# Performance work log

Hardware: AMD Instinct MI355X
Metric: run time of the kernel (lower is better)

Reference implementation:

```python
import jax, jax.numpy as jnp
import numpy as np

EMBEDDING_DIM = 256
WINDOW = 3


def setup_inputs() -> dict:
    key = jax.random.key(0)
    ks = jax.random.split(key, 7)
    B, T, F = 65536, 16, 129
    D = 64  # feature_dim = embedding_dim // 4 = cutoff = int(F*0.5)
    freq_history = jax.random.normal(ks[0], (B, T, F), dtype=jnp.float32)
    # pattern_detector: Linear(D, D) + LayerNorm(D) + GELU
    W1 = jax.random.normal(ks[1], (D, D), dtype=jnp.float32) * (1.0 / np.sqrt(D))
    b1 = jnp.zeros((D,), dtype=jnp.float32)
    gamma = jnp.ones((D,), dtype=jnp.float32)
    beta = jnp.zeros((D,), dtype=jnp.float32)
    # repetition_classifier: Linear(D, 1) + Sigmoid
    W2 = jax.random.normal(ks[2], (D, 1), dtype=jnp.float32) * (1.0 / np.sqrt(D))
    b2 = jnp.zeros((1,), dtype=jnp.float32)
    return {"freq_history": freq_history, "W1": W1, "b1": b1,
            "gamma": gamma, "beta": beta, "W2": W2, "b2": b2}


def reference(freq_history, W1, b1, gamma, beta, W2, b2):
    F = freq_history.shape[2]
    cutoff = int(F * 0.5)  # 64
    # keep last `window_size` steps
    fh = freq_history[:, -WINDOW:, :]  # [B, 3, F]
    # high-frequency magnitude: abs -> clamp -> per-sample standardize -> clamp
    hfm = jnp.clip(jnp.abs(fh[:, :, :cutoff]), 1e-5, 10.0)  # [B, 3, C]
    mean = hfm.mean(axis=(1, 2), keepdims=True)
    std = hfm.std(axis=(1, 2), keepdims=True, ddof=1) + 1e-5  # torch std is unbiased
    hfm = jnp.clip((hfm - mean) / std, -3.0, 3.0)
    # pattern detector on latest frame (dim_adapter is None: input_dim == feature_dim)
    latest = hfm[:, -1, :]  # [B, C]
    h = latest @ W1 + b1
    mu = h.mean(axis=-1, keepdims=True)
    var = h.var(axis=-1, keepdims=True)
    h = (h - mu) * jax.lax.rsqrt(var + 1e-5) * gamma + beta
    h = jax.nn.gelu(h, approximate=False)  # torch default GELU is exact erf
    repetition_scores = jax.nn.sigmoid(h @ W2 + b2)  # [B, 1]
    # DTW similarity: sequences passed have length 1 -> short-circuit branch:
    # dist = ||first - last||_2, similarity = exp(-dist / embedding_dim)
    diff = fh[:, 0, :cutoff] - fh[:, -1, :cutoff]  # [B, C]
    dist = jnp.sqrt(jnp.sum(diff * diff, axis=1))
    dtw_similarity = jnp.exp(-dist / EMBEDDING_DIM)[:, None]  # [B, 1]
    return repetition_scores, dtw_similarity
```

## Files before the change

kernel.cpp:

```cpp
#include <hip/hip_runtime.h>
#include <math.h>

#define TROWS 16
#define FFEAT 129
#define DD    64
#define TILE  64
#define LROW  72

typedef float f32x4 __attribute__((ext_vector_type(4)));
typedef short s16x8 __attribute__((ext_vector_type(8)));

__device__ __forceinline__ float lane_bcast(float v, int k) {
    return __uint_as_float(__builtin_amdgcn_readlane(__float_as_uint(v), k));
}

#define DPP_ADD(x, ctrl)                                                     \
    (x) += __int_as_float(__builtin_amdgcn_update_dpp(                       \
        0, __float_as_int(x), (ctrl), 0xf, 0xf, true))

#define WAVE_LADDER(x)                                                       \
    do {                                                                     \
        DPP_ADD(x, 0x111); DPP_ADD(x, 0x112); DPP_ADD(x, 0x114);             \
        DPP_ADD(x, 0x118); DPP_ADD(x, 0x142); DPP_ADD(x, 0x143);             \
    } while (0)

#define ROW_REDUCE(x)                                                        \
    do {                                                                     \
        DPP_ADD(x, 0x128); DPP_ADD(x, 0x124);                                \
        DPP_ADD(x, 0x122); DPP_ADD(x, 0x121);                                \
    } while (0)

__device__ __forceinline__ unsigned short f32_to_bf16(float f) {
    unsigned int u = __float_as_uint(f);
    return (unsigned short)((u + 0x7fffu + ((u >> 16) & 1u)) >> 16);
}

__global__ __launch_bounds__(256, 4) void dtw_tracker_kernel(
    const float* __restrict__ fh,
    const float* __restrict__ W1,
    const float* __restrict__ b1,
    const float* __restrict__ gamma,
    const float* __restrict__ beta,
    const float* __restrict__ W2,
    const float* __restrict__ b2,
    float* __restrict__ out,
    int nB)
{
    __shared__ unsigned short sLat[TILE * LROW];

    const int tid  = threadIdx.x;
    const int lane = tid & 63;
    const int wib  = tid >> 6;
    const int n0   = lane & 15;
    const int kg   = lane >> 4;

    s16x8 Bf[2][4];
    #pragma unroll
    for (int s = 0; s < 2; ++s) {
        #pragma unroll
        for (int t = 0; t < 4; ++t) {
            #pragma unroll
            for (int j = 0; j < 8; ++j) {
                const float w = W1[(s * 32 + kg * 8 + j) * DD + (n0 + 16 * t)];
                Bf[s][t][j] = (short)f32_to_bf16(w);
            }
        }
    }

    float b1v[4], gv[4], bv[4], w2v[4];
    #pragma unroll
    for (int t = 0; t < 4; ++t) {
        const int nt = n0 + 16 * t;
        b1v[t] = b1[nt]; gv[t] = gamma[nt]; bv[t] = beta[nt]; w2v[t] = W2[nt];
    }
    const float b2s = b2[0];

    const int bbase = blockIdx.x * TILE;
    const int bw    = bbase + wib * 16;
    const size_t rowOff = (size_t)13 * FFEAT + lane;

    const float* p0 = fh + (size_t)bw * (TROWS * FFEAT) + rowOff;
    float x13 = p0[0], x14 = p0[FFEAT], x15 = p0[2 * FFEAT];

    #pragma unroll 1
    for (int i = 0; i < 16; ++i) {
        const int inext = (i < 15) ? i + 1 : 15;
        const float* pn = fh + (size_t)(bw + inext) * (TROWS * FFEAT) + rowOff;
        const float y13 = pn[0], y14 = pn[FFEAT], y15 = pn[2 * FFEAT];

        const float c13 = fminf(fmaxf(fabsf(x13), 1e-5f), 10.0f);
        const float c14 = fminf(fmaxf(fabsf(x14), 1e-5f), 10.0f);
        const float c15 = fminf(fmaxf(fabsf(x15), 1e-5f), 10.0f);

        float s  = c13 + c14 + c15;
        float sq = fmaf(c13, c13, fmaf(c14, c14, c15 * c15));
        const float d0 = x13 - x15;
        float dd = d0 * d0;
        WAVE_LADDER(s); WAVE_LADDER(sq); WAVE_LADDER(dd);
        const float Ssum = lane_bcast(s, 63);
        const float SQs  = lane_bcast(sq, 63);
        const float DDs  = lane_bcast(dd, 63);

        const float mean = Ssum * (1.0f / 192.0f);
        float var = (SQs - Ssum * Ssum * (1.0f / 192.0f)) * (1.0f / 191.0f);
        var = fmaxf(var, 0.0f);
        const float stdv = sqrtf(var) + 1e-5f;
        const float latest =
            fminf(fmaxf(__fdividef(c15 - mean, stdv), -3.0f), 3.0f);

        sLat[(wib * 16 + i) * LROW + lane] = f32_to_bf16(latest);

        if (lane == 0)
            out[nB + (bw + i)] = __expf(-sqrtf(DDs) * (1.0f / 256.0f));

        x13 = y13; x14 = y14; x15 = y15;
    }

    const int r = wib * 16 + n0;
    const unsigned short* ar = &sLat[r * LROW + kg * 8];
    const s16x8 a0 = *(const s16x8*)(ar);
    const s16x8 a1 = *(const s16x8*)(ar + 32);

    f32x4 acc[4];
    #pragma unroll
    for (int t = 0; t < 4; ++t) {
        acc[t] = f32x4{0.0f, 0.0f, 0.0f, 0.0f};
        acc[t] = __builtin_amdgcn_mfma_f32_16x16x32_bf16(a0, Bf[0][t], acc[t], 0, 0, 0);
        acc[t] = __builtin_amdgcn_mfma_f32_16x16x32_bf16(a1, Bf[1][t], acc[t], 0, 0, 0);
    }

    #pragma unroll
    for (int q = 0; q < 4; ++q) {
        const float h0 = acc[0][q] + b1v[0];
        const float h1 = acc[1][q] + b1v[1];
        const float h2 = acc[2][q] + b1v[2];
        const float h3 = acc[3][q] + b1v[3];

        float s  = (h0 + h1) + (h2 + h3);
        float ss = fmaf(h0, h0, fmaf(h1, h1, fmaf(h2, h2, h3 * h3)));
        ROW_REDUCE(s); ROW_REDUCE(ss);

        const float mu = s * (1.0f / 64.0f);
        float vv = ss * (1.0f / 64.0f) - mu * mu;
        vv = fmaxf(vv, 0.0f);
        const float rstd = rsqrtf(vv + 1e-5f);

        float sc = 0.0f;
        #pragma unroll
        for (int t = 0; t < 4; ++t) {
            const float hv = (t == 0) ? h0 : (t == 1) ? h1 : (t == 2) ? h2 : h3;
            const float hn = (hv - mu) * rstd * gv[t] + bv[t];
            const float y  = 0.7978845608028654f *
                             fmaf(0.044715f * hn * hn, hn, hn);
            const float ey = __expf(2.0f * y);
            const float th = 1.0f - __fdividef(2.0f, ey + 1.0f);
            const float g  = 0.5f * hn * (1.0f + th);
            sc = fmaf(g, w2v[t], sc);
        }
        ROW_REDUCE(sc);

        const float rep = __fdividef(1.0f, 1.0f + __expf(-(sc + b2s)));
        if (n0 == q) {
            const int bidx = bbase + wib * 16 + kg * 4 + q;
            out[bidx] = rep;
        }
    }
}

extern "C" void kernel_launch(void* const* d_in, const int* in_sizes, int n_in,
                              void* d_out, int out_size, void* d_ws, size_t ws_size,
                              hipStream_t stream) {
    const float* fh    = (const float*)d_in[0];
    const float* W1    = (const float*)d_in[1];
    const float* b1    = (const float*)d_in[2];
    const float* gamma = (const float*)d_in[3];
    const float* beta  = (const float*)d_in[4];
    const float* W2    = (const float*)d_in[5];
    const float* b2    = (const float*)d_in[6];
    float* out = (float*)d_out;

    const int nB = in_sizes[0] / (TROWS * FFEAT);

    const int nBlocks = nB / TILE;
    dtw_tracker_kernel<<<nBlocks, 256, 0, stream>>>(fh, W1, b1, gamma, beta,
                                                    W2, b2, out, nB);
}
```

Before: 29.71 us.

## Process four samples per wave with 16-lane row reductions and permuted K layout

Restructures the statistics phase so each 16-lane row handles one sample with 12 values per lane, processing four samples per wave per iteration. Full-wave DPP ladders and readlane broadcasts become 16-lane row reductions. Loads are issued in fully unrolled batches of 12 for more memory-level parallelism. The latest-frame values are stored as packed 4-element bf16 writes in a permuted column order, and W1 rows are permuted to match, which adds register pressure and strided 16-element loads in exchange.

```diff
diff --git a/kernel.cpp b/kernel.cpp
--- a/kernel.cpp
+++ b/kernel.cpp
@@ -9,20 +9,11 @@
 
 typedef float f32x4 __attribute__((ext_vector_type(4)));
 typedef short s16x8 __attribute__((ext_vector_type(8)));
-
-__device__ __forceinline__ float lane_bcast(float v, int k) {
-    return __uint_as_float(__builtin_amdgcn_readlane(__float_as_uint(v), k));
-}
+typedef unsigned short u16x4 __attribute__((ext_vector_type(4)));
 
 #define DPP_ADD(x, ctrl)                                                     \
     (x) += __int_as_float(__builtin_amdgcn_update_dpp(                       \
         0, __float_as_int(x), (ctrl), 0xf, 0xf, true))
-
-#define WAVE_LADDER(x)                                                       \
-    do {                                                                     \
-        DPP_ADD(x, 0x111); DPP_ADD(x, 0x112); DPP_ADD(x, 0x114);             \
-        DPP_ADD(x, 0x118); DPP_ADD(x, 0x142); DPP_ADD(x, 0x143);             \
-    } while (0)
 
 #define ROW_REDUCE(x)                                                        \
     do {                                                                     \
@@ -33,6 +24,20 @@
 __device__ __forceinline__ unsigned short f32_to_bf16(float f) {
     unsigned int u = __float_as_uint(f);
     return (unsigned short)((u + 0x7fffu + ((u >> 16) & 1u)) >> 16);
+}
+
+__device__ __forceinline__ int kperm(int s) {
+    return (s >> 2) + ((s & 3) << 4);
+}
+
+__device__ __forceinline__ void load12(float v[12], const float* __restrict__ fh,
+                                       int b, int ll) {
+    const float* base = fh + (size_t)b * (TROWS * FFEAT) + 13 * FFEAT + ll;
+    #pragma unroll
+    for (int r = 0; r < 3; ++r)
+        #pragma unroll
+        for (int c = 0; c < 4; ++c)
+            v[r * 4 + c] = base[r * FFEAT + 16 * c];
 }
 
 __global__ __launch_bounds__(256, 4) void dtw_tracker_kernel(
@@ -56,13 +61,14 @@
 
     s16x8 Bf[2][4];
     #pragma unroll
-    for (int s = 0; s < 2; ++s) {
+    for (int h = 0; h < 2; ++h) {
         #pragma unroll
         for (int t = 0; t < 4; ++t) {
             #pragma unroll
             for (int j = 0; j < 8; ++j) {
-                const float w = W1[(s * 32 + kg * 8 + j) * DD + (n0 + 16 * t)];
-                Bf[s][t][j] = (short)f32_to_bf16(w);
+                const int s = h * 32 + kg * 8 + j;
+                const float w = W1[kperm(s) * DD + (n0 + 16 * t)];
+                Bf[h][t][j] = (short)f32_to_bf16(w);
             }
         }
     }
@@ -76,44 +82,53 @@
     const float b2s = b2[0];
 
     const int bbase = blockIdx.x * TILE;
-    const int bw    = bbase + wib * 16;
-    const size_t rowOff = (size_t)13 * FFEAT + lane;
-
-    const float* p0 = fh + (size_t)bw * (TROWS * FFEAT) + rowOff;
-    float x13 = p0[0], x14 = p0[FFEAT], x15 = p0[2 * FFEAT];
-
-    #pragma unroll 1
-    for (int i = 0; i < 16; ++i) {
-        const int inext = (i < 15) ? i + 1 : 15;
-        const float* pn = fh + (size_t)(bw + inext) * (TROWS * FFEAT) + rowOff;
-        const float y13 = pn[0], y14 = pn[FFEAT], y15 = pn[2 * FFEAT];
-
-        const float c13 = fminf(fmaxf(fabsf(x13), 1e-5f), 10.0f);
-        const float c14 = fminf(fmaxf(fabsf(x14), 1e-5f), 10.0f);
-        const float c15 = fminf(fmaxf(fabsf(x15), 1e-5f), 10.0f);
-
-        float s  = c13 + c14 + c15;
-        float sq = fmaf(c13, c13, fmaf(c14, c14, c15 * c15));
-        const float d0 = x13 - x15;
-        float dd = d0 * d0;
-        WAVE_LADDER(s); WAVE_LADDER(sq); WAVE_LADDER(dd);
-        const float Ssum = lane_bcast(s, 63);
-        const float SQs  = lane_bcast(sq, 63);
-        const float DDs  = lane_bcast(dd, 63);
-
-        const float mean = Ssum * (1.0f / 192.0f);
-        float var = (SQs - Ssum * Ssum * (1.0f / 192.0f)) * (1.0f / 191.0f);
+    const int wb    = bbase + wib * 16;
+    const int ll    = n0;
+    const int g     = kg;
+
+    float cur[12], nxt[12];
+    load12(cur, fh, wb + g, ll);
+
+    #pragma unroll
+    for (int i = 0; i < 4; ++i) {
+        if (i < 3) load12(nxt, fh, wb + 4 * (i + 1) + g, ll);
+
+        float cl[12];
+        #pragma unroll
+        for (int j = 0; j < 12; ++j)
+            cl[j] = fminf(fmaxf(fabsf(cur[j]), 1e-5f), 10.0f);
+
+        float s = 0.0f, sq = 0.0f, dd = 0.0f;
+        #pragma unroll
+        for (int j = 0; j < 12; ++j) { s += cl[j]; sq = fmaf(cl[j], cl[j], sq); }
+        #pragma unroll
+        for (int c = 0; c < 4; ++c) {
+            const float d = cur[c] - cur[8 + c];
+            dd = fmaf(d, d, dd);
+        }
+        ROW_REDUCE(s); ROW_REDUCE(sq); ROW_REDUCE(dd);
+
+        const float mean = s * (1.0f / 192.0f);
+        float var = (sq - s * s * (1.0f / 192.0f)) * (1.0f / 191.0f);
         var = fmaxf(var, 0.0f);
         const float stdv = sqrtf(var) + 1e-5f;
-        const float latest =
-            fminf(fmaxf(__fdividef(c15 - mean, stdv), -3.0f), 3.0f);
-
-        sLat[(wib * 16 + i) * LROW + lane] = f32_to_bf16(latest);
-
-        if (lane == 0)
-            out[nB + (bw + i)] = __expf(-sqrtf(DDs) * (1.0f / 256.0f));
-
-        x13 = y13; x14 = y14; x15 = y15;
+        const float rinv = __fdividef(1.0f, stdv);
+
+        u16x4 pk;
+        #pragma unroll
+        for (int c = 0; c < 4; ++c) {
+            const float lat =
+                fminf(fmaxf((cl[8 + c] - mean) * rinv, -3.0f), 3.0f);
+            pk[c] = f32_to_bf16(lat);
+        }
+        const int row = wib * 16 + 4 * i + g;
+        *(u16x4*)&sLat[row * LROW + ll * 4] = pk;
+
+        if (ll == 0)
+            out[nB + (wb + 4 * i + g)] = __expf(-sqrtf(dd) * (1.0f / 256.0f));
+
+        #pragma unroll
+        for (int j = 0; j < 12; ++j) cur[j] = nxt[j];
     }
 
     const int r = wib * 16 + n0;
@@ -154,8 +169,8 @@
                              fmaf(0.044715f * hn * hn, hn, hn);
             const float ey = __expf(2.0f * y);
             const float th = 1.0f - __fdividef(2.0f, ey + 1.0f);
-            const float g  = 0.5f * hn * (1.0f + th);
-            sc = fmaf(g, w2v[t], sc);
+            const float ge = 0.5f * hn * (1.0f + th);
+            sc = fmaf(ge, w2v[t], sc);
         }
         ROW_REDUCE(sc);
 
```

Measured after the change: 25.26 us, median of 2. 15.0% less time.
